# Kernel tuning notes

Measured on AMD Instinct MI355X. Metric: run time of the kernel, lower is better.

Reference implementation:

```python
import jax, jax.numpy as jnp
import numpy as np

D, H, HKV, HD = 1024, 16, 4, 64
ROPE_BASE = 10000.0
QK_GAIN_INIT = 1.0


def setup_inputs() -> dict:
    key = jax.random.key(0)
    ks = jax.random.split(key, 6)
    B, S = 2, 2048
    kv_dim = HKV * HD
    x = jax.random.normal(ks[0], (B, S, D), dtype=jnp.float32)
    Wq = jax.random.normal(ks[1], (D, D), dtype=jnp.float32) * 0.02
    Wk = jax.random.normal(ks[2], (kv_dim, D), dtype=jnp.float32) * 0.02
    Wv = jax.random.normal(ks[3], (kv_dim, D), dtype=jnp.float32) * 0.02
    Wo = jax.random.normal(ks[4], (D, D), dtype=jnp.float32) * 0.02
    q_gain = jnp.full((H,), QK_GAIN_INIT, dtype=jnp.float32)
    return {"x": x, "Wq": Wq, "Wk": Wk, "Wv": Wv, "Wo": Wo, "q_gain": q_gain}


def _rms_norm(t):
    eps = jnp.finfo(t.dtype).eps
    return t * jax.lax.rsqrt(jnp.mean(t * t, axis=-1, keepdims=True) + eps)


def _rope(t, cos, sin):
    # t: [B,h,S,HD]; cos/sin: [1,1,S,HD//2]
    half = t.shape[-1] // 2
    t1, t2 = t[..., :half], t[..., half:]
    return jnp.concatenate((t1 * cos + t2 * sin, -t1 * sin + t2 * cos), axis=-1)


def _attention(x, Wq, Wk, Wv, Wo, q_gain):
    B, S, _ = x.shape
    q = (x @ Wq.T).reshape(B, S, H, HD).transpose(0, 2, 1, 3)     # [B,H,S,HD]
    k = (x @ Wk.T).reshape(B, S, HKV, HD).transpose(0, 2, 1, 3)   # [B,HKV,S,HD]
    v = (x @ Wv.T).reshape(B, S, HKV, HD).transpose(0, 2, 1, 3)
    q, k = _rms_norm(q), _rms_norm(k)
    # rotary tables
    inv_freq = 1.0 / (ROPE_BASE ** (jnp.arange(0, HD, 2, dtype=jnp.float32) / HD))
    freqs = jnp.arange(S, dtype=jnp.float32)[:, None] * inv_freq[None, :]  # [S,HD//2]
    cos, sin = jnp.cos(freqs)[None, None], jnp.sin(freqs)[None, None]
    q, k = _rope(q, cos, sin), _rope(k, cos, sin)
    q = q * q_gain[None, :, None, None]
    # GQA: repeat kv heads to match query heads
    g = H // HKV
    k = jnp.repeat(k, g, axis=1)
    v = jnp.repeat(v, g, axis=1)
    scale = 1.0 / jnp.sqrt(jnp.asarray(HD, q.dtype))
    scores = jnp.einsum('bhqd,bhkd->bhqk', q, k) * scale
    causal = jnp.tril(jnp.ones((S, S), dtype=bool))
    scores = jnp.where(causal[None, None], scores, jnp.asarray(-jnp.inf, scores.dtype))
    attn = jax.nn.softmax(scores, axis=-1)
    y = jnp.einsum('bhqk,bhkd->bhqd', attn, v)                    # [B,H,S,HD]
    y = y.transpose(0, 2, 1, 3).reshape(B, S, D)
    return y @ Wo.T


def reference(x, Wq, Wk, Wv, Wo, q_gain):
    return _attention(x, Wq, Wk, Wv, Wo, q_gain)
```

## Files before the change

### kernel.cpp

```cpp
#include <hip/hip_runtime.h>
#include <hip/hip_bf16.h>
#include <math.h>

typedef __attribute__((ext_vector_type(8))) __bf16 bf16x8;
typedef __attribute__((ext_vector_type(4))) short short4v;
typedef __attribute__((ext_vector_type(4))) float f32x4;
typedef __attribute__((ext_vector_type(4))) unsigned short ushort4v;
typedef __attribute__((ext_vector_type(8))) unsigned short ushort8;

#define LOG2E 1.44269504088896340736f

static __device__ __forceinline__ unsigned short f2bf(float f) {
  unsigned int u = __float_as_uint(f);
  return (unsigned short)((u + 0x7fffu + ((u >> 16) & 1u)) >> 16);
}
static __device__ __forceinline__ short bfbits(float f) {
  __bf16 h = (__bf16)f;
  return __builtin_bit_cast(short, h);
}

static __device__ __forceinline__ void gload16(const unsigned short* g, void* l) {
  __builtin_amdgcn_global_load_lds(
      (const __attribute__((address_space(1))) unsigned int*)g,
      (__attribute__((address_space(3))) unsigned int*)l, 16, 0, 0);
}

__global__ __launch_bounds__(256) void prep_kernel(
    const float* __restrict__ x, const float* __restrict__ Wq,
    const float* __restrict__ Wk, const float* __restrict__ Wv,
    const float* __restrict__ Wo,
    unsigned short* __restrict__ xb, unsigned short* __restrict__ wqkv,
    unsigned short* __restrict__ wo_b, float* __restrict__ tab) {
  const int bx = blockIdx.x, tid = threadIdx.x;
  if (bx < 6656) {
    const float* src;
    unsigned short* dst;
    int i;
    if (bx < 4096)       { src = x;  dst = xb;             i = bx * 256 + tid; }
    else if (bx < 5120)  { src = Wq; dst = wqkv;           i = (bx - 4096) * 256 + tid; }
    else if (bx < 5376)  { src = Wk; dst = wqkv + 1048576; i = (bx - 5120) * 256 + tid; }
    else if (bx < 5632)  { src = Wv; dst = wqkv + 1310720; i = (bx - 5376) * 256 + tid; }
    else                 { src = Wo; dst = wo_b;           i = (bx - 5632) * 256 + tid; }
    float4 v = reinterpret_cast<const float4*>(src)[i];
    ushort4v o;
    o.x = f2bf(v.x); o.y = f2bf(v.y); o.z = f2bf(v.z); o.w = f2bf(v.w);
    reinterpret_cast<ushort4v*>(dst)[i] = o;
  } else {
    int i = (bx - 6656) * 256 + tid;
    int s = i >> 5, d = i & 31;
    float invf = powf(10000.f, -(float)d / 32.f);
    float fr = (float)s * invf;
    tab[s * 64 + d] = cosf(fr);
    tab[s * 64 + 32 + d] = sinf(fr);
  }
}

__global__ __launch_bounds__(256) void gemm_qkv_kernel(
    const unsigned short* __restrict__ A, const unsigned short* __restrict__ B,
    const float* __restrict__ tab, const float* __restrict__ qg,
    unsigned short* __restrict__ qb, unsigned short* __restrict__ kb,
    unsigned short* __restrict__ vsl) {
  __shared__ unsigned short sA[64 * 64];
  __shared__ unsigned short sB[128 * 64];
  const int t = threadIdx.x;
  const int lane = t & 63;
  const int w = t >> 6;
  const int bm = blockIdx.x / 12, bn = blockIdx.x % 12;
  const long m0 = (long)bm * 64, n0 = (long)bn * 128;
  const int wm = (w >> 1) * 32, wn = (w & 1) * 64;
  const int lr = lane & 15, lg = lane >> 4;
  f32x4 acc[2][4];
#pragma unroll
  for (int i = 0; i < 2; i++)
#pragma unroll
    for (int j = 0; j < 4; j++) acc[i][j] = (f32x4){0.f, 0.f, 0.f, 0.f};

  for (int k0 = 0; k0 < 1024; k0 += 64) {
#pragma unroll
    for (int i = 0; i < 2; i++) {
      int chunk = i * 256 + t;
      int r = chunk >> 3;
      int c = (chunk & 7) << 3;
      gload16(A + (m0 + r) * 1024 + k0 + c, (char*)sA + chunk * 16);
    }
#pragma unroll
    for (int i = 0; i < 4; i++) {
      int chunk = i * 256 + t;
      int r = chunk >> 3;
      int c = (chunk & 7) << 3;
      gload16(B + (n0 + r) * 1024 + k0 + c, (char*)sB + chunk * 16);
    }
    __syncthreads();
#pragma unroll
    for (int kk = 0; kk < 2; ++kk) {
      bf16x8 af[2], bfr[4];
#pragma unroll
      for (int m = 0; m < 2; m++)
        af[m] = *(const bf16x8*)&sA[(wm + m * 16 + lr) * 64 + kk * 32 + lg * 8];
#pragma unroll
      for (int n = 0; n < 4; n++)
        bfr[n] = *(const bf16x8*)&sB[(wn + n * 16 + lr) * 64 + kk * 32 + lg * 8];
#pragma unroll
      for (int m = 0; m < 2; m++)
#pragma unroll
        for (int n = 0; n < 4; n++)
          acc[m][n] = __builtin_amdgcn_mfma_f32_16x16x32_bf16(af[m], bfr[n], acc[m][n], 0, 0, 0);
    }
    __syncthreads();
  }
  const int bb = (int)(m0 >> 11);
  const int s_base = (int)(m0 & 2047) + wm + lg * 4;
  const int hsel = wn >> 6;
  if (bn < 10) {
    float gscale = 1.0f;
    unsigned short* dstb;
    if (bn < 8) {
      gscale = qg[2 * bn + hsel] * (0.125f * LOG2E);
      dstb = qb + (size_t)(bb * 16 + 2 * bn + hsel) * 2048 * 64;
    } else {
      dstb = kb + (size_t)(bb * 4 + 2 * (bn - 8) + hsel) * 2048 * 64;
    }
#pragma unroll
    for (int m = 0; m < 2; m++) {
#pragma unroll
      for (int j = 0; j < 4; j++) {
        float ss = acc[m][0][j] * acc[m][0][j] + acc[m][1][j] * acc[m][1][j] +
                   acc[m][2][j] * acc[m][2][j] + acc[m][3][j] * acc[m][3][j];
        ss += __shfl_xor(ss, 1);
        ss += __shfl_xor(ss, 2);
        ss += __shfl_xor(ss, 4);
        ss += __shfl_xor(ss, 8);
        const float rinv = rsqrtf(ss * (1.0f / 64.0f) + 1.1920929e-07f);
        const int s = s_base + m * 16 + j;
        const float* tr = tab + s * 64;
        const float c0 = tr[lr], c1 = tr[16 + lr];
        const float s0 = tr[32 + lr], s1 = tr[48 + lr];
        const float n0v = acc[m][0][j] * rinv, n1v = acc[m][1][j] * rinv;
        const float n2v = acc[m][2][j] * rinv, n3v = acc[m][3][j] * rinv;
        float o0 = (n0v * c0 + n2v * s0) * gscale;
        float o1 = (n1v * c1 + n3v * s1) * gscale;
        float o2 = (n2v * c0 - n0v * s0) * gscale;
        float o3 = (n3v * c1 - n1v * s1) * gscale;
        unsigned short* d = dstb + (size_t)s * 64;
        d[lr]      = f2bf(o0);
        d[16 + lr] = f2bf(o1);
        d[32 + lr] = f2bf(o2);
        d[48 + lr] = f2bf(o3);
      }
    }
  } else {
#pragma unroll
    for (int m = 0; m < 2; m++) {
#pragma unroll
      for (int j = 0; j < 4; j++) {
        const int s = s_base + m * 16 + j;
        unsigned short* d = vsl + (size_t)(bb * 2048 + s) * 256 + (bn - 10) * 128 + wn;
#pragma unroll
        for (int n = 0; n < 4; n++) d[n * 16 + lr] = f2bf(acc[m][n][j]);
      }
    }
  }
}

__global__ __launch_bounds__(256) void gemm_bt_kernel(
    const unsigned short* __restrict__ A, const unsigned short* __restrict__ B,
    float* __restrict__ C, int M, int N, int K, int nbn) {
  __shared__ unsigned short sA[64 * 64];
  __shared__ unsigned short sB[128 * 64];
  const int t = threadIdx.x;
  const int lane = t & 63;
  const int w = t >> 6;
  const int bm = blockIdx.x / nbn, bn = blockIdx.x % nbn;
  const long m0 = (long)bm * 64, n0 = (long)bn * 128;
  const int wm = (w >> 1) * 32, wn = (w & 1) * 64;
  const int lr = lane & 15, lg = lane >> 4;
  f32x4 acc[2][4];
#pragma unroll
  for (int i = 0; i < 2; i++)
#pragma unroll
    for (int j = 0; j < 4; j++) acc[i][j] = (f32x4){0.f, 0.f, 0.f, 0.f};

  for (int k0 = 0; k0 < K; k0 += 64) {
#pragma unroll
    for (int i = 0; i < 2; i++) {
      int chunk = i * 256 + t;
      int r = chunk >> 3;
      int c = (chunk & 7) << 3;
      gload16(A + (m0 + r) * (long)K + k0 + c, (char*)sA + chunk * 16);
    }
#pragma unroll
    for (int i = 0; i < 4; i++) {
      int chunk = i * 256 + t;
      int r = chunk >> 3;
      int c = (chunk & 7) << 3;
      gload16(B + (n0 + r) * (long)K + k0 + c, (char*)sB + chunk * 16);
    }
    __syncthreads();
#pragma unroll
    for (int kk = 0; kk < 2; ++kk) {
      bf16x8 af[2], bfr[4];
#pragma unroll
      for (int m = 0; m < 2; m++)
        af[m] = *(const bf16x8*)&sA[(wm + m * 16 + lr) * 64 + kk * 32 + lg * 8];
#pragma unroll
      for (int n = 0; n < 4; n++)
        bfr[n] = *(const bf16x8*)&sB[(wn + n * 16 + lr) * 64 + kk * 32 + lg * 8];
#pragma unroll
      for (int m = 0; m < 2; m++)
#pragma unroll
        for (int n = 0; n < 4; n++)
          acc[m][n] = __builtin_amdgcn_mfma_f32_16x16x32_bf16(af[m], bfr[n], acc[m][n], 0, 0, 0);
    }
    __syncthreads();
  }
#pragma unroll
  for (int m = 0; m < 2; m++) {
#pragma unroll
    for (int n = 0; n < 4; n++) {
      long col = n0 + wn + n * 16 + lr;
#pragma unroll
      for (int j = 0; j < 4; j++) {
        long row = m0 + wm + m * 16 + lg * 4 + j;
        C[row * N + col] = acc[m][n][j];
      }
    }
  }
}

__global__ __launch_bounds__(256) void vpack_kernel(
    const unsigned short* __restrict__ vsl, unsigned short* __restrict__ vtb) {
  __shared__ unsigned short sT[64 * 65];
  const int tid = threadIdx.x;
  const int bhk = blockIdx.x >> 5;
  const int st = blockIdx.x & 31;
  const int b = bhk >> 2, hk = bhk & 3;
  const int r = tid >> 2, cg = (tid & 3) << 4;
  const unsigned short* src = vsl + (size_t)(b * 2048 + st * 64 + r) * 256 + hk * 64 + cg;
  ushort8 v0 = *(const ushort8*)src;
  ushort8 v1 = *(const ushort8*)(src + 8);
#pragma unroll
  for (int k = 0; k < 8; ++k) sT[r * 65 + cg + k] = v0[k];
#pragma unroll
  for (int k = 0; k < 8; ++k) sT[r * 65 + cg + 8 + k] = v1[k];
  __syncthreads();
  const int d = tid >> 2, sg = (tid & 3) << 4;
  ushort8 o0, o1;
#pragma unroll
  for (int k = 0; k < 8; ++k) o0[k] = sT[(sg + k) * 65 + d];
#pragma unroll
  for (int k = 0; k < 8; ++k) o1[k] = sT[(sg + 8 + k) * 65 + d];
  unsigned short* dst = vtb + ((size_t)(bhk * 64 + d)) * 2048 + st * 64 + sg;
  *(ushort8*)dst = o0;
  *(ushort8*)(dst + 8) = o1;
}

__global__ __launch_bounds__(256) void attn_kernel(
    const unsigned short* __restrict__ qb, const unsigned short* __restrict__ kb,
    const unsigned short* __restrict__ vtb, unsigned short* __restrict__ yb,
    const float* __restrict__ qg) {
  __shared__ unsigned short sK[2][64 * 64];
  __shared__ unsigned short sV[2][64 * 64];
  const int tid = threadIdx.x;
  const int lane = tid & 63;
  const int w = tid >> 6;
  const int qt = 31 - (blockIdx.x >> 5);
  const int bh = blockIdx.x & 31;
  const int h = bh & 15;
  const int b = bh >> 4;
  const float M = 11.7f * fabsf(qg[h]);
  const int q0 = qt * 64 + w * 16;
  const unsigned short* Q  = qb  + (size_t)(b * 16 + h) * 2048 * 64;
  const unsigned short* Kp = kb  + (size_t)(b * 4 + (h >> 2)) * 2048 * 64;
  const unsigned short* Vp = vtb + (size_t)(b * 4 + (h >> 2)) * 64 * 2048;
  const int qc = lane & 15;
  const int g = lane >> 4;
  const int qrow = q0 + qc;
  const bf16x8 qf0 = *(const bf16x8*)(Q + (size_t)qrow * 64 + g * 8);
  const bf16x8 qf1 = *(const bf16x8*)(Q + (size_t)qrow * 64 + 32 + g * 8);
  f32x4 acc[4];
  acc[0] = acc[1] = acc[2] = acc[3] = (f32x4){0.f, 0.f, 0.f, 0.f};
  float lsum = 0.f;
  const int nt = qt + 1;

  const int r0 = tid >> 3, c0 = tid & 7;
  const int swz = ((c0 ^ (r0 & 7)) << 3);
  const unsigned short* gK = Kp + (size_t)r0 * 64 + swz;
  const unsigned short* gV = Vp + (size_t)r0 * 2048 + swz;

  gload16(gK,             (char*)&sK[0][0] + tid * 16);
  gload16(gK + 32 * 64,   (char*)&sK[0][0] + (tid + 256) * 16);
  gload16(gV,             (char*)&sV[0][0] + tid * 16);
  gload16(gV + 32 * 2048, (char*)&sV[0][0] + (tid + 256) * 16);
  gK += 64 * 64; gV += 64;

  int cur = 0;
  for (int t = 0; t < nt; ++t) {
    __syncthreads();
    if (t + 1 < nt) {
      const int nb = cur ^ 1;
      gload16(gK,             (char*)&sK[nb][0] + tid * 16);
      gload16(gK + 32 * 64,   (char*)&sK[nb][0] + (tid + 256) * 16);
      gload16(gV,             (char*)&sV[nb][0] + tid * 16);
      gload16(gV + 32 * 2048, (char*)&sV[nb][0] + (tid + 256) * 16);
      gK += 64 * 64; gV += 64;
    }
    const unsigned short* sKc = &sK[cur][0];
    const unsigned short* sVc = &sV[cur][0];
    f32x4 st[4];
    __builtin_amdgcn_s_setprio(1);
#pragma unroll
    for (int ks = 0; ks < 4; ++ks) {
      const int rr = ks * 16 + qc;
      bf16x8 kf0 = *(const bf16x8*)&sKc[rr * 64 + ((g ^ (rr & 7)) << 3)];
      bf16x8 kf1 = *(const bf16x8*)&sKc[rr * 64 + (((4 + g) ^ (rr & 7)) << 3)];
      f32x4 a = (f32x4){0.f, 0.f, 0.f, 0.f};
      a = __builtin_amdgcn_mfma_f32_16x16x32_bf16(kf0, qf0, a, 0, 0, 0);
      a = __builtin_amdgcn_mfma_f32_16x16x32_bf16(kf1, qf1, a, 0, 0, 0);
      st[ks] = a;
    }
    __builtin_amdgcn_s_setprio(0);
    if (t == nt - 1) {
#pragma unroll
      for (int ks = 0; ks < 4; ++ks)
#pragma unroll
        for (int j = 0; j < 4; ++j)
          if (ks * 16 + g * 4 + j > w * 16 + qc) st[ks][j] = -1e30f;
    }
    short4v pb[4];
#pragma unroll
    for (int ks = 0; ks < 4; ++ks)
#pragma unroll
      for (int j = 0; j < 4; ++j) {
        float p = exp2f(st[ks][j] - M);
        lsum += p;
        pb[ks][j] = bfbits(p);
      }
    __builtin_amdgcn_s_setprio(1);
#pragma unroll
    for (int ks = 0; ks < 4; ++ks) {
#pragma unroll
      for (int d = 0; d < 4; ++d) {
        const int rd = d * 16 + qc;
        const int el = rd * 64 + ((((ks * 2 + (g >> 1)) ^ (rd & 7)) << 3) + ((g & 1) << 2));
        short4v vf = *(const short4v*)&sVc[el];
        acc[d] = __builtin_amdgcn_mfma_f32_16x16x16bf16_1k(vf, pb[ks], acc[d], 0, 0, 0);
      }
    }
    __builtin_amdgcn_s_setprio(0);
    cur ^= 1;
  }
  float l = lsum;
  l += __shfl_xor(l, 16);
  l += __shfl_xor(l, 32);
  const float inv = 1.0f / l;
  unsigned short* Y = yb + (size_t)(b * 2048 + qrow) * 1024 + h * 64;
#pragma unroll
  for (int d = 0; d < 4; ++d)
#pragma unroll
    for (int j = 0; j < 4; ++j)
      Y[d * 16 + g * 4 + j] = (unsigned short)bfbits(acc[d][j] * inv);
}

extern "C" void kernel_launch(void* const* d_in, const int* in_sizes, int n_in,
                              void* d_out, int out_size, void* d_ws, size_t ws_size,
                              hipStream_t stream) {
  const float* x  = (const float*)d_in[0];
  const float* Wq = (const float*)d_in[1];
  const float* Wk = (const float*)d_in[2];
  const float* Wv = (const float*)d_in[3];
  const float* Wo = (const float*)d_in[4];
  const float* qg = (const float*)d_in[5];
  float* out = (float*)d_out;

  char* ws = (char*)d_ws;
  const size_t NEED = 37224448;
  if (ws_size < NEED) return;
  unsigned short* xb   = (unsigned short*)(ws);
  unsigned short* wqkv = (unsigned short*)(ws + 8388608);
  unsigned short* wo_b = (unsigned short*)(ws + 11534336);
  unsigned short* vsl  = (unsigned short*)(ws + 13631488);
  unsigned short* qbuf = (unsigned short*)(ws + 15728640);
  unsigned short* kbuf = (unsigned short*)(ws + 24117248);
  unsigned short* vtb  = (unsigned short*)(ws + 26214400);
  unsigned short* ybuf = (unsigned short*)(ws + 28311552);
  float*          tab  = (float*)        (ws + 36700160);

  prep_kernel<<<6912, 256, 0, stream>>>(x, Wq, Wk, Wv, Wo, xb, wqkv, wo_b, tab);
  gemm_qkv_kernel<<<64 * 12, 256, 0, stream>>>(xb, wqkv, tab, qg, qbuf, kbuf, vsl);
  vpack_kernel<<<256, 256, 0, stream>>>(vsl, vtb);
  attn_kernel<<<1024, 256, 0, stream>>>(qbuf, kbuf, vtb, ybuf, qg);
  gemm_bt_kernel<<<64 * 8, 256, 0, stream>>>(ybuf, wo_b, out, 4096, 1024, 1024, 8);
}
```

Measured before the change: 108.0 us.

## Fuse V transpose into QKV GEMM epilogue and vectorize attention output stores

The QKV GEMM epilogue for V blocks now stages the tile in shared memory and writes V directly in the transposed per-head layout, which removes the separate vpack kernel and its intermediate buffer. This saves one launch and a full round trip of V through global memory. The attention kernel's output store is also packed into 4-element vector writes. The cost is an extra __syncthreads and some LDS transpose work in the V blocks of the GEMM.

After: 105.3 us. 1.03x faster.

```diff
diff --git a/kernel.cpp b/kernel.cpp
--- a/kernel.cpp
+++ b/kernel.cpp
@@ -59,9 +59,10 @@
     const unsigned short* __restrict__ A, const unsigned short* __restrict__ B,
     const float* __restrict__ tab, const float* __restrict__ qg,
     unsigned short* __restrict__ qb, unsigned short* __restrict__ kb,
-    unsigned short* __restrict__ vsl) {
-  __shared__ unsigned short sA[64 * 64];
-  __shared__ unsigned short sB[128 * 64];
+    unsigned short* __restrict__ vtb) {
+  __shared__ unsigned short sAll[64 * 64 + 128 * 64];
+  unsigned short* sA = sAll;
+  unsigned short* sB = sAll + 64 * 64;
   const int t = threadIdx.x;
   const int lane = t & 63;
   const int w = t >> 6;
@@ -149,15 +150,29 @@
       }
     }
   } else {
-#pragma unroll
-    for (int m = 0; m < 2; m++) {
+    unsigned short* sT = sAll;
+#pragma unroll
+    for (int m = 0; m < 2; m++)
 #pragma unroll
       for (int j = 0; j < 4; j++) {
-        const int s = s_base + m * 16 + j;
-        unsigned short* d = vsl + (size_t)(bb * 2048 + s) * 256 + (bn - 10) * 128 + wn;
-#pragma unroll
-        for (int n = 0; n < 4; n++) d[n * 16 + lr] = f2bf(acc[m][n][j]);
-      }
+        const int srow = wm + m * 16 + lg * 4 + j;
+#pragma unroll
+        for (int n = 0; n < 4; n++)
+          sT[(hsel * 64 + srow) * 72 + n * 16 + lr] = f2bf(acc[m][n][j]);
+      }
+    __syncthreads();
+    const int hd = t >> 7;
+    const int d  = (t >> 1) & 63;
+    const int sh = t & 1;
+    const int hk = 2 * (bn - 10) + hd;
+    unsigned short* dst = vtb + ((size_t)((bb * 4 + hk) * 64 + d)) * 2048 +
+                          (int)(m0 & 2047) + sh * 32;
+    ushort8 o;
+#pragma unroll
+    for (int c = 0; c < 4; ++c) {
+#pragma unroll
+      for (int k = 0; k < 8; ++k) o[k] = sT[(hd * 64 + sh * 32 + c * 8 + k) * 72 + d];
+      *(ushort8*)(dst + c * 8) = o;
     }
   }
 }
@@ -225,33 +240,6 @@
       }
     }
   }
-}
-
-__global__ __launch_bounds__(256) void vpack_kernel(
-    const unsigned short* __restrict__ vsl, unsigned short* __restrict__ vtb) {
-  __shared__ unsigned short sT[64 * 65];
-  const int tid = threadIdx.x;
-  const int bhk = blockIdx.x >> 5;
-  const int st = blockIdx.x & 31;
-  const int b = bhk >> 2, hk = bhk & 3;
-  const int r = tid >> 2, cg = (tid & 3) << 4;
-  const unsigned short* src = vsl + (size_t)(b * 2048 + st * 64 + r) * 256 + hk * 64 + cg;
-  ushort8 v0 = *(const ushort8*)src;
-  ushort8 v1 = *(const ushort8*)(src + 8);
-#pragma unroll
-  for (int k = 0; k < 8; ++k) sT[r * 65 + cg + k] = v0[k];
-#pragma unroll
-  for (int k = 0; k < 8; ++k) sT[r * 65 + cg + 8 + k] = v1[k];
-  __syncthreads();
-  const int d = tid >> 2, sg = (tid & 3) << 4;
-  ushort8 o0, o1;
-#pragma unroll
-  for (int k = 0; k < 8; ++k) o0[k] = sT[(sg + k) * 65 + d];
-#pragma unroll
-  for (int k = 0; k < 8; ++k) o1[k] = sT[(sg + 8 + k) * 65 + d];
-  unsigned short* dst = vtb + ((size_t)(bhk * 64 + d)) * 2048 + st * 64 + sg;
-  *(ushort8*)dst = o0;
-  *(ushort8*)(dst + 8) = o1;
 }
 
 __global__ __launch_bounds__(256) void attn_kernel(
@@ -355,10 +343,12 @@
   const float inv = 1.0f / l;
   unsigned short* Y = yb + (size_t)(b * 2048 + qrow) * 1024 + h * 64;
 #pragma unroll
-  for (int d = 0; d < 4; ++d)
-#pragma unroll
-    for (int j = 0; j < 4; ++j)
-      Y[d * 16 + g * 4 + j] = (unsigned short)bfbits(acc[d][j] * inv);
+  for (int d = 0; d < 4; ++d) {
+    ushort4v o;
+#pragma unroll
+    for (int j = 0; j < 4; ++j) o[j] = (unsigned short)bfbits(acc[d][j] * inv);
+    *(ushort4v*)(Y + d * 16 + g * 4) = o;
+  }
 }
 
 extern "C" void kernel_launch(void* const* d_in, const int* in_sizes, int n_in,
@@ -373,21 +363,19 @@
   float* out = (float*)d_out;
 
   char* ws = (char*)d_ws;
-  const size_t NEED = 37224448;
+  const size_t NEED = 35127296;
   if (ws_size < NEED) return;
   unsigned short* xb   = (unsigned short*)(ws);
   unsigned short* wqkv = (unsigned short*)(ws + 8388608);
   unsigned short* wo_b = (unsigned short*)(ws + 11534336);
-  unsigned short* vsl  = (unsigned short*)(ws + 13631488);
-  unsigned short* qbuf = (unsigned short*)(ws + 15728640);
-  unsigned short* kbuf = (unsigned short*)(ws + 24117248);
-  unsigned short* vtb  = (unsigned short*)(ws + 26214400);
-  unsigned short* ybuf = (unsigned short*)(ws + 28311552);
-  float*          tab  = (float*)        (ws + 36700160);
+  unsigned short* qbuf = (unsigned short*)(ws + 13631488);
+  unsigned short* kbuf = (unsigned short*)(ws + 22020096);
+  unsigned short* vtb  = (unsigned short*)(ws + 24117248);
+  unsigned short* ybuf = (unsigned short*)(ws + 26214400);
+  float*          tab  = (float*)        (ws + 34603008);
 
   prep_kernel<<<6912, 256, 0, stream>>>(x, Wq, Wk, Wv, Wo, xb, wqkv, wo_b, tab);
-  gemm_qkv_kernel<<<64 * 12, 256, 0, stream>>>(xb, wqkv, tab, qg, qbuf, kbuf, vsl);
-  vpack_kernel<<<256, 256, 0, stream>>>(vsl, vtb);
+  gemm_qkv_kernel<<<64 * 12, 256, 0, stream>>>(xb, wqkv, tab, qg, qbuf, kbuf, vtb);
   attn_kernel<<<1024, 256, 0, stream>>>(qbuf, kbuf, vtb, ybuf, qg);
   gemm_bt_kernel<<<64 * 8, 256, 0, stream>>>(ybuf, wo_b, out, 4096, 1024, 1024, 8);
 }
```
